# Optimization experiments

Measured on AMD Instinct MI355X. Metric: run time of the kernel, lower is better.

The kernel has to match this reference:

```python
import jax, jax.numpy as jnp
import numpy as np

# dims matching input_specs / init_kwargs
S_BATCH, T_BATCH, NUM, DIM, H, W = 4, 4, 8, 512, 32, 32
K = 64              # self.k, number of kmeans clusters
KMEANS_ITERS = 10   # fixed Lloyd iterations (stand-in for kmeans-to-convergence)


def _kmeans(points):
    """Euclidean Lloyd kmeans. points: [n, d] -> centers [K, d].
    Deterministic init: first K points. Empty clusters keep old center."""
    centers0 = points[:K]
    sq_p = jnp.sum(points * points, axis=1)  # [n]

    def step(centers, _):
        # squared euclidean distance [n, K]
        d2 = sq_p[:, None] + jnp.sum(centers * centers, axis=1)[None, :] \
             - 2.0 * points @ centers.T
        assign = jnp.argmin(d2, axis=1)                      # [n]
        onehot = jax.nn.one_hot(assign, K, dtype=points.dtype)  # [n, K]
        counts = onehot.sum(axis=0)                          # [K]
        sums = onehot.T @ points                             # [K, d]
        new = jnp.where(counts[:, None] > 0,
                        sums / jnp.maximum(counts, 1.0)[:, None],
                        centers)
        return new, None

    centers, _ = jax.lax.scan(step, centers0, None, length=KMEANS_ITERS)
    return centers


def setup_inputs() -> dict:
    key = jax.random.key(0)
    k1, k2, k3, k4 = jax.random.split(key, 4)
    return {
        "source_feat": jax.random.normal(k1, (S_BATCH, NUM, DIM, H, W), dtype=jnp.float32),
        "target_feat": jax.random.normal(k2, (T_BATCH, NUM, DIM, H, W), dtype=jnp.float32),
        "source_label": jax.random.randint(k3, (S_BATCH,), 0, 10),
        "target_label": jax.random.randint(k4, (T_BATCH,), 0, 10),
    }


def reference(source_feat, target_feat, source_label, target_label):
    sb, num, dim, h, w = source_feat.shape
    tb = target_feat.shape[0]

    # view each map as (h*w, dim) point cloud, kmeans per (batch, num)
    s_pts = source_feat.reshape(sb, num, dim, h * w).transpose(0, 1, 3, 2)
    t_pts = target_feat.reshape(tb, num, dim, h * w).transpose(0, 1, 3, 2)
    km = jax.vmap(jax.vmap(_kmeans))
    cs = km(s_pts).transpose(1, 0, 2, 3)  # [num, sb, K, dim]
    ct = km(t_pts).transpose(1, 0, 2, 3)  # [num, tb, K, dim]

    # mat_dist for every (num, i, j) pair of center sets: [num, sb, tb, K, K]
    sq_s = jnp.sum(cs * cs, axis=-1)  # [num, sb, K]
    sq_t = jnp.sum(ct * ct, axis=-1)  # [num, tb, K]
    dots = jnp.einsum('nikd,njld->nijkl', cs, ct)
    dist = jnp.sqrt(jnp.maximum(
        sq_s[:, :, None, :, None] + sq_t[:, None, :, None, :] - 2.0 * dots, 0.0))
    y = jnp.argmin(dist, axis=-1)  # [num, sb, tb, K] nearest target center per source center

    # gather matched target centers; replicate source centers over j (torch append order: i, j, k)
    ct_b = jnp.broadcast_to(ct[:, None], (num, sb, tb, K, dim))
    t_mat = jnp.take_along_axis(ct_b, y[..., None], axis=3)            # [num, sb, tb, K, dim]
    s_mat = jnp.broadcast_to(cs[:, :, None], (num, sb, tb, K, dim))

    N = sb * tb * K
    s_mat = s_mat.reshape(num, N, dim)
    t_mat = t_mat.reshape(num, N, dim)

    # trans_mat[k] = s_mat.T @ pinv(t_mat.T)   -> [num, dim, dim]
    pinv_t = jnp.linalg.pinv(t_mat.transpose(0, 2, 1))  # pinv([dim, N]) -> [num, N, dim]
    trans_mat = jnp.einsum('nkd,nke->nde', s_mat, pinv_t)
    return trans_mat
```

## Files before the change

kernel.cpp:

```cpp
#include <hip/hip_runtime.h>

typedef unsigned int u32;
typedef unsigned long long u64;

#define NPTS  1024
#define DIMD  512
#define KCL   64
#define KMIT  10

constexpr size_t O_CTG  = 0;
constexpr size_t O_SUMS = O_CTG  + 64ull*512*64;
constexpr size_t O_CNT  = O_SUMS + 64ull*64*512;
constexpr size_t O_SQC  = O_CNT  + 64ull*64;
constexpr size_t O_SQP  = O_SQC  + 64ull*64;
constexpr size_t O_ASG  = O_SQP  + 64ull*1024;
constexpr size_t O_CTN  = O_ASG  + 64ull*1024;
constexpr size_t O_Y    = O_CTN  + 8ull*256*512;
constexpr size_t O_CNT2 = O_Y    + 8ull*4*4*64;
constexpr size_t O_BM   = O_CNT2 + 8ull*256;
constexpr size_t O_G    = O_BM   + 8ull*256*512;
constexpr size_t O_LT   = O_G    + 8ull*256*256;
constexpr size_t O_YB   = O_LT   + 8ull*256*256;
constexpr size_t O_ZB   = O_YB   + 8ull*256*512;
constexpr size_t O_PTST = O_ZB   + 8ull*256*512;

constexpr size_t O_PS0 = O_SUMS;
constexpr size_t O_PS1 = O_CTN;
static_assert(O_PS1 + 64ull*64*512 <= O_G, "PS1 overlay must fit before O_G");

constexpr size_t O_BEST = O_G;

constexpr size_t O_CS = O_SUMS;
constexpr size_t O_W  = O_YB;
constexpr size_t O_WT = O_YB + 8ull*4*64*64;

__device__ __forceinline__ const float* run_base(const float* s, const float* t, int run){
    const float* b = (run < 32) ? s : t;
    return b + (size_t)(run & 31) * (DIMD * NPTS);
}
__device__ __forceinline__ u64 dpack(float d2, int c){
    u32 u = __float_as_uint(d2);
    u = (u & 0x80000000u) ? ~u : (u | 0x80000000u);
    return ((u64)u << 32) | (u32)c;
}
__device__ __forceinline__ float rdlane(float v, int l){
    return __uint_as_float(__builtin_amdgcn_readlane(__float_as_uint(v), l));
}

__global__ __launch_bounds__(256) void k_init(const float* __restrict__ src, const float* __restrict__ tgt,
                                              float* __restrict__ ws){
    int bx = blockIdx.x; int run = bx >> 2, q = bx & 3;
    int tid = threadIdx.x;
    const float* base = run_base(src, tgt, run);
    int p = q*256 + tid;
    float acc = 0.f;
    for (int d = 0; d < DIMD; ++d){
        float v = base[(size_t)d*NPTS + p];
        acc = fmaf(v, v, acc);
    }
    ws[O_SQP + run*NPTS + p] = acc;
    if (q == 0){
        if (tid < KCL) ws[O_SQC + run*KCL + tid] = acc;
        if (tid < KCL) ((int*)(ws + O_CNT))[run*KCL + tid] = 0;
        for (int idx = tid; idx < DIMD*KCL; idx += 256){
            int d = idx >> 6, c = idx & 63;
            ws[O_CTG + (size_t)run*DIMD*KCL + idx] = base[(size_t)d*NPTS + c];
        }
    }
}

__global__ __launch_bounds__(256) void k_ptsT(const float* __restrict__ src, const float* __restrict__ tgt,
                                              float* __restrict__ ws){
    int bx = blockIdx.x; int dt = bx & 7, pt = (bx >> 3) & 15, run = bx >> 7;
    int tid = threadIdx.x, lane = tid & 63, r4 = tid >> 6;
    const float* base = run_base(src, tgt, run);
    __shared__ float t[64*65];
    for (int pass = 0; pass < 16; ++pass){
        int r = pass*4 + r4;
        t[r*65 + lane] = base[(size_t)(dt*64 + r)*NPTS + pt*64 + lane];
    }
    __syncthreads();
    for (int pass = 0; pass < 16; ++pass){
        int p = pass*4 + r4;
        ws[O_PTST + ((size_t)run*NPTS + pt*64 + p)*DIMD + dt*64 + lane] = t[lane*65 + p];
    }
}

__global__ __launch_bounds__(256, 4) void k_assign(const float* __restrict__ src, const float* __restrict__ tgt,
                                                   const float* __restrict__ ctr, const float* __restrict__ sqc,
                                                   const float* __restrict__ sqp,
                                                   u64* __restrict__ bestg){
    int bxx = blockIdx.x;
    int cb  = (bxx >> 3) & 1;
    int w   = ((bxx >> 4) << 3) | (bxx & 7);
    int run = w >> 3, qt = w & 7;
    int tid = threadIdx.x, lane = tid & 63;
    int g = __builtin_amdgcn_readfirstlane(tid >> 6);
    int c0 = cb*32 + g*8;
    const float* base = run_base(src, tgt, run);
    const float* cg = ctr + (size_t)run*DIMD*KCL + c0;
    int p0 = qt*128 + 2*lane;
    float acc[2][8] = {};
    __shared__ u64 red[4][128];

#define LOADP(P, B) { \
    _Pragma("unroll") \
    for (int u = 0; u < 16; ++u) \
        P[u] = *(const float2*)&base[(size_t)((B)*16 + u)*NPTS + p0]; }

#define COMPUTE(P, B) { \
    _Pragma("unroll") \
    for (int u = 0; u < 16; ++u){ \
        const float4* cp = (const float4*)(cg + (size_t)((B)*16 + u)*KCL); \
        float4 c0v = cp[0], c1v = cp[1]; \
        float cv[8] = {c0v.x,c0v.y,c0v.z,c0v.w, c1v.x,c1v.y,c1v.z,c1v.w}; \
        _Pragma("unroll") \
        for (int cl = 0; cl < 8; ++cl){ \
            acc[0][cl] = fmaf(P[u].x, cv[cl], acc[0][cl]); \
            acc[1][cl] = fmaf(P[u].y, cv[cl], acc[1][cl]); \
        } \
    } }

    float2 pa[16], pb[16];
    LOADP(pa, 0);
    for (int b = 0; b < 32; b += 2){
        if (b + 1 < 32) LOADP(pb, b + 1);
        COMPUTE(pa, b);
        if (b + 2 < 32) LOADP(pa, b + 2);
        COMPUTE(pb, b + 1);
    }
#undef LOADP
#undef COMPUTE

    const float* sqcg = sqc + run*KCL + c0;
    float sq[8];
    #pragma unroll
    for (int q = 0; q < 8; ++q) sq[q] = sqcg[q];
    float2 sq2 = *(const float2*)&sqp[run*NPTS + p0];
    #pragma unroll
    for (int s = 0; s < 2; ++s){
        float sqpv = s ? sq2.y : sq2.x;
        u64 best = dpack(sqpv + sq[0] - 2.f*acc[s][0], c0);
        #pragma unroll
        for (int cl = 1; cl < 8; ++cl){
            u64 k2 = dpack(sqpv + sq[cl] - 2.f*acc[s][cl], c0 + cl);
            best = (k2 < best) ? k2 : best;
        }
        red[g][2*lane + s] = best;
    }
    __syncthreads();
    if (tid < 128){
        u64 b = red[0][tid];
        #pragma unroll
        for (int g2 = 1; g2 < 4; ++g2){ u64 k2 = red[g2][tid]; b = (k2 < b) ? k2 : b; }
        bestg[(((size_t)(run*8 + qt)*128 + tid) << 1) + cb] = b;
    }
}

__global__ __launch_bounds__(256) void k_sums(float* __restrict__ ws){
    int bx = blockIdx.x; int pg = bx & 1, dh = (bx >> 1) & 1, run = bx >> 2;
    int tid = threadIdx.x;
    __shared__ float sm[KCL*256];
    __shared__ int a[512];
    const u64* bestg = (const u64*)(ws + O_BEST);
    int* cnt = (int*)(ws + O_CNT);
    for (int idx = tid; idx < 512; idx += 256){
        int p = pg*512 + idx;
        int qt = p >> 7, t = p & 127;
        const u64* bp = bestg + (((size_t)(run*8 + qt)*128 + t) << 1);
        u64 x = bp[0], y = bp[1];
        u64 m = (y < x) ? y : x;
        int c = (int)(m & 0xffffffffu);
        a[idx] = c;
        if (dh == 0) atomicAdd(&cnt[run*KCL + c], 1);
    }
    for (int idx = tid; idx < KCL*256; idx += 256) sm[idx] = 0.f;
    __syncthreads();
    const float* pT = ws + O_PTST + ((size_t)run*NPTS + pg*512)*DIMD + dh*256 + tid;
    for (int p = 0; p < 512; p += 4){
        float v0 = pT[(size_t)(p+0)*DIMD], v1 = pT[(size_t)(p+1)*DIMD];
        float v2 = pT[(size_t)(p+2)*DIMD], v3 = pT[(size_t)(p+3)*DIMD];
        sm[a[p+0]*256 + tid] += v0;
        sm[a[p+1]*256 + tid] += v1;
        sm[a[p+2]*256 + tid] += v2;
        sm[a[p+3]*256 + tid] += v3;
    }
    __syncthreads();
    size_t psx = pg ? O_PS1 : O_PS0;
    for (int c = 0; c < KCL; ++c)
        ws[psx + ((size_t)run*KCL + c)*DIMD + dh*256 + tid] = sm[c*256 + tid];
}

__global__ __launch_bounds__(256) void k_newc(float* __restrict__ ws){
    int run = blockIdx.x, tid = threadIdx.x;
    __shared__ float sm2[KCL*65];
    __shared__ int cl[KCL];
    int* cnt = (int*)(ws + O_CNT);
    if (tid < KCL) cl[tid] = cnt[run*KCL + tid];
    __syncthreads();
    if (tid < KCL) cnt[run*KCL + tid] = 0;
    float sqa = 0.f;
    for (int dc = 0; dc < 8; ++dc){
        for (int idx = tid; idx < KCL*64; idx += 256){
            int c = idx >> 6, dl = idx & 63;
            size_t o = ((size_t)run*KCL + c)*DIMD + dc*64 + dl;
            sm2[c*65 + dl] = ws[O_PS0 + o] + ws[O_PS1 + o];
        }
        __syncthreads();
        for (int idx = tid; idx < KCL*64; idx += 256){
            int dl = idx >> 6, c = idx & 63, d = dc*64 + dl;
            size_t gi = O_CTG + (size_t)run*DIMD*KCL + d*KCL + c;
            float old = ws[gi];
            int cc = cl[c];
            float nv = (cc > 0) ? sm2[c*65 + dl] / (float)cc : old;
            ws[gi] = nv;
            sm2[c*65 + dl] = nv;
        }
        __syncthreads();
        if (tid < KCL){
            for (int dl = 0; dl < 64; ++dl){ float v = sm2[tid*65 + dl]; sqa = fmaf(v, v, sqa); }
        }
        __syncthreads();
    }
    if (tid < KCL) ws[O_SQC + run*KCL + tid] = sqa;
}

__global__ __launch_bounds__(256) void k_ctn(float* __restrict__ ws){
    int bx = blockIdx.x; int dc = bx & 7, jj = (bx >> 3) & 3, n = (bx >> 5) & 7, st = bx >> 8;
    int run = st ? (jj*8 + n) : (32 + jj*8 + n);
    int tid = threadIdx.x, lane = tid & 63, r4 = tid >> 6;
    __shared__ float t[64*65];
    for (int pass = 0; pass < 16; ++pass){
        int r = pass*4 + r4;
        t[r*65 + lane] = ws[O_CTG + (size_t)run*DIMD*KCL + (dc*64 + r)*KCL + lane];
    }
    __syncthreads();
    size_t dstbase = st ? (O_CS  + ((size_t)(n*4 + jj)*64)*DIMD)
                        : (O_CTN + ((size_t)n*256 + jj*64)*DIMD);
    for (int pass = 0; pass < 16; ++pass){
        int l = pass*4 + r4;
        ws[dstbase + (size_t)l*DIMD + dc*64 + lane] = t[lane*65 + l];
    }
}

__global__ __launch_bounds__(256) void k_map(float* __restrict__ ws){
    int bx = blockIdx.x; int j = bx & 3, i = (bx >> 2) & 3, n = bx >> 4;
    int run_s = i*8 + n, run_t = 32 + j*8 + n;
    int tid = threadIdx.x, lane = tid & 63;
    int g = __builtin_amdgcn_readfirstlane(tid >> 6);
    const float* cgs = ws + O_CTG + (size_t)run_s*DIMD*KCL + lane;
    const float* cgt = ws + O_CTG + (size_t)run_t*DIMD*KCL + g*16;
    float acc[16] = {};
    for (int d = 0; d < DIMD; ++d){
        float csv = cgs[d*KCL];
        const float4* cp = (const float4*)(cgt + d*KCL);
        float4 c0=cp[0], c1=cp[1], c2=cp[2], c3=cp[3];
        float cv[16] = {c0.x,c0.y,c0.z,c0.w, c1.x,c1.y,c1.z,c1.w,
                        c2.x,c2.y,c2.z,c2.w, c3.x,c3.y,c3.z,c3.w};
        #pragma unroll
        for (int cl = 0; cl < 16; ++cl) acc[cl] = fmaf(csv, cv[cl], acc[cl]);
    }
    float sqs = ws[O_SQC + run_s*KCL + lane];
    const float* sqtp = ws + O_SQC + run_t*KCL + g*16;
    u64 best = dpack(sqs + sqtp[0] - 2.f*acc[0], g*16);
    #pragma unroll
    for (int cl = 1; cl < 16; ++cl){
        u64 k2 = dpack(sqs + sqtp[cl] - 2.f*acc[cl], g*16 + cl);
        best = (k2 < best) ? k2 : best;
    }
    __shared__ u64 red[4][64];
    red[g][lane] = best;
    __syncthreads();
    if (tid < 64){
        u64 b = red[0][tid];
        #pragma unroll
        for (int g2 = 1; g2 < 4; ++g2){ u64 k2 = red[g2][tid]; b = (k2 < b) ? k2 : b; }
        int l = (int)(b & 0xffffffffu);
        int* yv   = (int*)(ws + O_Y);
        int* cnt2 = (int*)(ws + O_CNT2);
        yv[((n*4 + i)*4 + j)*64 + tid] = l;
        atomicAdd(&cnt2[n*256 + j*64 + l], 1);
    }
}

__global__ __launch_bounds__(256) void k_bmat(float* __restrict__ ws){
    int bx = blockIdx.x; int dh = bx & 1, j = (bx >> 1) & 3, n = bx >> 3;
    int tid = threadIdx.x;
    __shared__ float Bacc[KCL*256];
    __shared__ int yl[256];
    __shared__ int c2[KCL];
    const int* yv   = (const int*)(ws + O_Y);
    const int* cnt2 = (const int*)(ws + O_CNT2);
    { int i = tid >> 6, k = tid & 63; yl[tid] = yv[((n*4 + i)*4 + j)*64 + k]; }
    if (tid < KCL) c2[tid] = cnt2[n*256 + j*64 + tid];
    for (int idx = tid; idx < KCL*256; idx += 256) Bacc[idx] = 0.f;
    __syncthreads();
    const float* cs = ws + O_CS + (size_t)(n*4)*64*DIMD + dh*256 + tid;
    #pragma unroll 4
    for (int s = 0; s < 256; ++s){
        int l = yl[s];
        float v = cs[(size_t)s*DIMD];
        Bacc[l*256 + tid] += v;
    }
    __syncthreads();
    for (int l = 0; l < KCL; ++l){
        int cc = c2[l]; if (cc < 1) cc = 1;
        ws[O_BM + ((size_t)n*256 + j*64 + l)*DIMD + dh*256 + tid] = Bacc[l*256 + tid] / (float)cc;
    }
}

__global__ __launch_bounds__(256) void k_gram(float* __restrict__ ws){
    int bx = blockIdx.x; int cc = bx & 7, n = bx >> 3;
    int tid = threadIdx.x, llane = tid & 63, jlane = tid >> 6;
    int run_t = 32 + jlane*8 + n;
    const float* bbase = ws + O_CTG + (size_t)run_t*DIMD*KCL + llane;
    const float* arow  = ws + O_CTN + (size_t)(n*256 + cc*32)*DIMD;
    float acc[32] = {};
    for (int d = 0; d < DIMD; d += 4){
        float bv0 = bbase[(d+0)*KCL], bv1 = bbase[(d+1)*KCL];
        float bv2 = bbase[(d+2)*KCL], bv3 = bbase[(d+3)*KCL];
        #pragma unroll
        for (int c = 0; c < 32; ++c){
            const float4 av = *(const float4*)&arow[c*DIMD + d];
            acc[c] = fmaf(av.x, bv0, acc[c]);
            acc[c] = fmaf(av.y, bv1, acc[c]);
            acc[c] = fmaf(av.z, bv2, acc[c]);
            acc[c] = fmaf(av.w, bv3, acc[c]);
        }
    }
    const int* cnt2 = (const int*)(ws + O_CNT2);
    bool used_cp = cnt2[n*256 + tid] > 0;
    float* Gp = ws + O_G + (size_t)n*65536;
    #pragma unroll
    for (int c = 0; c < 32; ++c){
        int cg = cc*32 + c;
        bool used_c = cnt2[n*256 + cg] > 0;
        float v = (used_c && used_cp) ? acc[c] : ((cg == tid) ? 1.f : 0.f);
        Gp[(size_t)cg*256 + tid] = v;
    }
}

__global__ __launch_bounds__(256, 1) void k_cholp(float* __restrict__ ws, int kb){
    int n = blockIdx.x, tid = threadIdx.x;
    int lane = tid & 63, wv = tid >> 6;
    float* Gn  = ws + O_G  + (size_t)n*65536;
    float* LTn = ws + O_LT + (size_t)n*65536;
    int c0 = kb*64, r1 = c0 + 64, rem = 256 - r1;

    float dreg[64];
    {
        const float* grow = Gn + (size_t)(c0+lane)*256 + c0;
        #pragma unroll
        for (int j4 = 0; j4 < 16; ++j4){
            float4 v = *(const float4*)&grow[j4*4];
            dreg[j4*4+0]=v.x; dreg[j4*4+1]=v.y; dreg[j4*4+2]=v.z; dreg[j4*4+3]=v.w;
        }
    }
    float preg[64];
    int prow = (wv-1)*64 + lane;
    bool pact = (wv >= 1) && (prow < rem);
    {
        const float* growp = Gn + (size_t)(r1+prow)*256 + c0;
        #pragma unroll
        for (int j4 = 0; j4 < 16; ++j4){
            if (pact){
                float4 v = *(const float4*)&growp[j4*4];
                preg[j4*4+0]=v.x; preg[j4*4+1]=v.y; preg[j4*4+2]=v.z; preg[j4*4+3]=v.w;
            } else {
                preg[j4*4+0]=0.f; preg[j4*4+1]=0.f; preg[j4*4+2]=0.f; preg[j4*4+3]=0.f;
            }
        }
    }
    #pragma unroll
    for (int k = 0; k < 64; ++k){
        float dkk = sqrtf(fmaxf(rdlane(dreg[k], k), 1e-30f));
        float inv = 1.f / dkk;
        dreg[k] = (lane == k) ? dkk : dreg[k]*inv;
        preg[k] *= inv;
        #pragma unroll
        for (int j = k+1; j < 64; ++j){
            float s = rdlane(dreg[k], j);
            dreg[j] = fmaf(-dreg[k], s, dreg[j]);
            preg[j] = fmaf(-preg[k], s, preg[j]);
        }
    }
    if (wv == 0){
        float* grow = Gn + (size_t)(c0+lane)*256 + c0;
        #pragma unroll
        for (int j4 = 0; j4 < 16; ++j4){
            float4 v; v.x=dreg[j4*4+0]; v.y=dreg[j4*4+1]; v.z=dreg[j4*4+2]; v.w=dreg[j4*4+3];
            *(float4*)&grow[j4*4] = v;
        }
    }
    if (pact){
        float* growp = Gn + (size_t)(r1+prow)*256 + c0;
        #pragma unroll
        for (int j4 = 0; j4 < 16; ++j4){
            float4 v; v.x=preg[j4*4+0]; v.y=preg[j4*4+1]; v.z=preg[j4*4+2]; v.w=preg[j4*4+3];
            *(float4*)&growp[j4*4] = v;
        }
        float* ltp = LTn + (size_t)c0*256 + r1 + prow;
        #pragma unroll
        for (int j = 0; j < 64; ++j) ltp[(size_t)j*256] = preg[j];
    }
}

__global__ __launch_bounds__(256) void k_trail(float* __restrict__ ws, int kb){
    int n = blockIdx.y;
    int c0 = kb*64, r1 = c0 + 64, rem = 256 - r1;
    int nt4 = rem >> 2;
    int ntiles = nt4*(nt4+1)/2;
    float* Gn = ws + O_G + (size_t)n*65536;
    for (int t = blockIdx.x*256 + threadIdx.x; t < ntiles; t += gridDim.x*256){
        int ti = (int)((sqrtf(8.f*(float)t + 1.f) - 1.f) * 0.5f);
        while ((ti+1)*(ti+2)/2 <= t) ++ti;
        while (ti*(ti+1)/2 > t) --ti;
        int tj = t - ti*(ti+1)/2;
        int i0 = ti*4, j0 = tj*4;
        const float* Li = Gn + (size_t)(r1+i0)*256 + c0;
        const float* Lj = Gn + (size_t)(r1+j0)*256 + c0;
        float acc[4][4] = {};
        for (int k = 0; k < 64; k += 4){
            float4 ar4[4], br4[4];
            #pragma unroll
            for (int r = 0; r < 4; ++r) ar4[r] = *(const float4*)&Li[(size_t)r*256 + k];
            #pragma unroll
            for (int s = 0; s < 4; ++s) br4[s] = *(const float4*)&Lj[(size_t)s*256 + k];
            #pragma unroll
            for (int q = 0; q < 4; ++q){
                float aq[4] = { q==0?ar4[0].x:q==1?ar4[0].y:q==2?ar4[0].z:ar4[0].w,
                                q==0?ar4[1].x:q==1?ar4[1].y:q==2?ar4[1].z:ar4[1].w,
                                q==0?ar4[2].x:q==1?ar4[2].y:q==2?ar4[2].z:ar4[2].w,
                                q==0?ar4[3].x:q==1?ar4[3].y:q==2?ar4[3].z:ar4[3].w };
                float bq[4] = { q==0?br4[0].x:q==1?br4[0].y:q==2?br4[0].z:br4[0].w,
                                q==0?br4[1].x:q==1?br4[1].y:q==2?br4[1].z:br4[1].w,
                                q==0?br4[2].x:q==1?br4[2].y:q==2?br4[2].z:br4[2].w,
                                q==0?br4[3].x:q==1?br4[3].y:q==2?br4[3].z:br4[3].w };
                #pragma unroll
                for (int r = 0; r < 4; ++r)
                    #pragma unroll
                    for (int s = 0; s < 4; ++s)
                        acc[r][s] = fmaf(aq[r], bq[s], acc[r][s]);
            }
        }
        #pragma unroll
        for (int r = 0; r < 4; ++r){
            float* grow = Gn + (size_t)(r1+i0+r)*256 + r1 + j0;
            #pragma unroll
            for (int s = 0; s < 4; ++s) grow[s] -= acc[r][s];
        }
    }
}

__global__ __launch_bounds__(256, 1) void k_dinv(float* __restrict__ ws){
    int n = blockIdx.x, tid = threadIdx.x;
    int lane = tid & 63, kb = tid >> 6;
    const float* Gn = ws + O_G + (size_t)n*65536;
    __shared__ __align__(16) float DlT[4][64*65];
    for (int idx = lane; idx < 1024; idx += 64){
        int r = idx >> 4, c4 = idx & 15;
        float4 v = *(const float4*)&Gn[(size_t)(kb*64 + r)*256 + kb*64 + c4*4];
        DlT[kb][(c4*4+0)*65 + r] = v.x;
        DlT[kb][(c4*4+1)*65 + r] = v.y;
        DlT[kb][(c4*4+2)*65 + r] = v.z;
        DlT[kb][(c4*4+3)*65 + r] = v.w;
    }
    __syncthreads();
    float x[64];
    #pragma unroll
    for (int i = 0; i < 64; ++i) x[i] = (i == lane) ? 1.f : 0.f;
    const float* Dk = DlT[kb];
    #pragma unroll
    for (int k = 0; k < 64; ++k){
        float invd = 1.f / Dk[k*65 + k];
        x[k] *= invd;
        #pragma unroll
        for (int i = k+1; i < 64; ++i)
            x[i] = fmaf(-Dk[k*65 + i], x[k], x[i]);
    }
    float* Wg  = ws + O_W  + ((size_t)n*4 + kb)*4096;
    float* WTg = ws + O_WT + ((size_t)n*4 + kb)*4096;
    #pragma unroll
    for (int r = 0; r < 64; ++r) Wg[r*64 + lane] = x[r];
    #pragma unroll
    for (int r4 = 0; r4 < 16; ++r4){
        float4 v; v.x=x[r4*4+0]; v.y=x[r4*4+1]; v.z=x[r4*4+2]; v.w=x[r4*4+3];
        *(float4*)&WTg[lane*64 + r4*4] = v;
    }
}

__global__ __launch_bounds__(256, 1) void k_solve(float* __restrict__ ws){
    int n = blockIdx.x, cg = blockIdx.y;
    int tid = threadIdx.x;
    int tx = tid & 15, ty = tid >> 4;
    const float* Gn  = ws + O_G  + (size_t)n*65536;
    const float* LTn = ws + O_LT + (size_t)n*65536;
    const float* Ct  = ws + O_CTN + (size_t)n*256*DIMD + (size_t)cg*64;
    const float* Wg  = ws + O_W  + (size_t)n*4*4096;
    const float* WTg = ws + O_WT + (size_t)n*4*4096;
    float* Zb = ws + O_ZB + (size_t)n*256*DIMD + (size_t)cg*64;

    __shared__ __align__(16) float YL[4][64*65];
    __shared__ __align__(16) float At[64*65];
    __shared__ __align__(16) float RL[64*65];

    float acc[4][4];
    for (int bi = 0; bi < 4; ++bi){
        #pragma unroll
        for (int a = 0; a < 4; ++a){
            float4 v = *(const float4*)&Ct[(size_t)(bi*64 + ty*4 + a)*DIMD + tx*4];
            acc[a][0]=v.x; acc[a][1]=v.y; acc[a][2]=v.z; acc[a][3]=v.w;
        }
        for (int j = 0; j < bi; ++j){
            __syncthreads();
            for (int idx = tid; idx < 1024; idx += 256){
                int k = idx >> 4, r4 = idx & 15;
                float4 v = *(const float4*)&LTn[(size_t)(j*64 + k)*256 + bi*64 + r4*4];
                *(float4*)&At[k*65 + r4*4] = v;
            }
            __syncthreads();
            const float* Yj = YL[j];
            #pragma unroll 8
            for (int k = 0; k < 64; ++k){
                float4 av = *(const float4*)&At[k*65 + ty*4];
                float4 yv = *(const float4*)&Yj[k*65 + tx*4];
                float ar[4] = {av.x,av.y,av.z,av.w};
                float yr[4] = {yv.x,yv.y,yv.z,yv.w};
                #pragma unroll
                for (int a = 0; a < 4; ++a)
                    #pragma unroll
                    for (int b = 0; b < 4; ++b)
                        acc[a][b] = fmaf(-ar[a], yr[b], acc[a][b]);
            }
        }
        __syncthreads();
        #pragma unroll
        for (int a = 0; a < 4; ++a){
            float4 v; v.x=acc[a][0]; v.y=acc[a][1]; v.z=acc[a][2]; v.w=acc[a][3];
            *(float4*)&RL[(ty*4 + a)*65 + tx*4] = v;
        }
        for (int idx = tid; idx < 1024; idx += 256){
            int k = idx >> 4, r4 = idx & 15;
            float4 v = *(const float4*)&WTg[(size_t)bi*4096 + k*64 + r4*4];
            *(float4*)&At[k*65 + r4*4] = v;
        }
        __syncthreads();
        float out[4][4] = {};
        #pragma unroll 8
        for (int k = 0; k < 64; ++k){
            float4 av = *(const float4*)&At[k*65 + ty*4];
            float4 rv = *(const float4*)&RL[k*65 + tx*4];
            float ar[4] = {av.x,av.y,av.z,av.w};
            float rr[4] = {rv.x,rv.y,rv.z,rv.w};
            #pragma unroll
            for (int a = 0; a < 4; ++a)
                #pragma unroll
                for (int b = 0; b < 4; ++b)
                    out[a][b] = fmaf(ar[a], rr[b], out[a][b]);
        }
        float* Yi = YL[bi];
        #pragma unroll
        for (int a = 0; a < 4; ++a){
            float4 v; v.x=out[a][0]; v.y=out[a][1]; v.z=out[a][2]; v.w=out[a][3];
            *(float4*)&Yi[(ty*4 + a)*65 + tx*4] = v;
        }
    }
    for (int bi = 3; bi >= 0; --bi){
        __syncthreads();
        #pragma unroll
        for (int a = 0; a < 4; ++a){
            float4 v = *(const float4*)&YL[bi][(ty*4 + a)*65 + tx*4];
            acc[a][0]=v.x; acc[a][1]=v.y; acc[a][2]=v.z; acc[a][3]=v.w;
        }
        for (int j = bi+1; j < 4; ++j){
            __syncthreads();
            for (int idx = tid; idx < 1024; idx += 256){
                int k = idx >> 4, r4 = idx & 15;
                float4 v = *(const float4*)&Gn[(size_t)(j*64 + k)*256 + bi*64 + r4*4];
                *(float4*)&At[k*65 + r4*4] = v;
            }
            __syncthreads();
            const float* Zj = YL[j];
            #pragma unroll 8
            for (int k = 0; k < 64; ++k){
                float4 av = *(const float4*)&At[k*65 + ty*4];
                float4 zv = *(const float4*)&Zj[k*65 + tx*4];
                float ar[4] = {av.x,av.y,av.z,av.w};
                float zr[4] = {zv.x,zv.y,zv.z,zv.w};
                #pragma unroll
                for (int a = 0; a < 4; ++a)
                    #pragma unroll
                    for (int b = 0; b < 4; ++b)
                        acc[a][b] = fmaf(-ar[a], zr[b], acc[a][b]);
            }
        }
        __syncthreads();
        #pragma unroll
        for (int a = 0; a < 4; ++a){
            float4 v; v.x=acc[a][0]; v.y=acc[a][1]; v.z=acc[a][2]; v.w=acc[a][3];
            *(float4*)&RL[(ty*4 + a)*65 + tx*4] = v;
        }
        for (int idx = tid; idx < 1024; idx += 256){
            int k = idx >> 4, r4 = idx & 15;
            float4 v = *(const float4*)&Wg[(size_t)bi*4096 + k*64 + r4*4];
            *(float4*)&At[k*65 + r4*4] = v;
        }
        __syncthreads();
        float out[4][4] = {};
        #pragma unroll 8
        for (int k = 0; k < 64; ++k){
            float4 av = *(const float4*)&At[k*65 + ty*4];
            float4 rv = *(const float4*)&RL[k*65 + tx*4];
            float ar[4] = {av.x,av.y,av.z,av.w};
            float rr[4] = {rv.x,rv.y,rv.z,rv.w};
            #pragma unroll
            for (int a = 0; a < 4; ++a)
                #pragma unroll
                for (int b = 0; b < 4; ++b)
                    out[a][b] = fmaf(ar[a], rr[b], out[a][b]);
        }
        float* Zi = YL[bi];
        #pragma unroll
        for (int a = 0; a < 4; ++a){
            float4 v; v.x=out[a][0]; v.y=out[a][1]; v.z=out[a][2]; v.w=out[a][3];
            *(float4*)&Zi[(ty*4 + a)*65 + tx*4] = v;
            *(float4*)&Zb[(size_t)(bi*64 + ty*4 + a)*DIMD + tx*4] = v;
        }
    }
}

__global__ __launch_bounds__(256) void k_gemmE(const float* __restrict__ ws, float* __restrict__ out){
    int bx = blockIdx.x; int et = bx & 7, dt = (bx >> 3) & 7, n = bx >> 6;
    int tid = threadIdx.x;
    __shared__ float Bl[256*64];
    __shared__ float Zl[256*64];
    const float* Bm = ws + O_BM + (size_t)n*256*DIMD;
    const float* Zb = ws + O_ZB + (size_t)n*256*DIMD;
    for (int idx = tid; idx < 16384; idx += 256){
        int c = idx >> 6, dd = idx & 63;
        Bl[idx] = Bm[(size_t)c*DIMD + dt*64 + dd];
        Zl[idx] = Zb[(size_t)c*DIMD + et*64 + dd];
    }
    __syncthreads();
    int td = tid & 15, te = tid >> 4;
    float acc[4][4] = {};
    for (int c = 0; c < 256; ++c){
        float4 bv = *(const float4*)&Bl[c*64 + td*4];
        float4 zv = *(const float4*)&Zl[c*64 + te*4];
        float b4[4] = {bv.x, bv.y, bv.z, bv.w};
        float z4[4] = {zv.x, zv.y, zv.z, zv.w};
        #pragma unroll
        for (int r = 0; r < 4; ++r)
            #pragma unroll
            for (int s = 0; s < 4; ++s) acc[r][s] = fmaf(b4[r], z4[s], acc[r][s]);
    }
    float* ob = out + (size_t)n*262144 + (size_t)(dt*64 + td*4)*DIMD + et*64 + te*4;
    #pragma unroll
    for (int r = 0; r < 4; ++r){
        float4 o; o.x = acc[r][0]; o.y = acc[r][1]; o.z = acc[r][2]; o.w = acc[r][3];
        *(float4*)&ob[(size_t)r*DIMD] = o;
    }
}

extern "C" void kernel_launch(void* const* d_in, const int* in_sizes, int n_in,
                              void* d_out, int out_size, void* d_ws, size_t ws_size,
                              hipStream_t stream){
    const float* src = (const float*)d_in[0];
    const float* tgt = (const float*)d_in[1];
    float* ws  = (float*)d_ws;
    float* out = (float*)d_out;

    k_init<<<256, 256, 0, stream>>>(src, tgt, ws);
    k_ptsT<<<8192, 256, 0, stream>>>(src, tgt, ws);

    for (int it = 0; it < KMIT; ++it){
        k_assign<<<1024, 256, 0, stream>>>(src, tgt,
                                           ws + O_CTG, ws + O_SQC, ws + O_SQP,
                                           (u64*)(ws + O_BEST));
        k_sums<<<256, 256, 0, stream>>>(ws);
        k_newc<<<64, 256, 0, stream>>>(ws);
    }

    hipMemsetAsync((char*)d_ws + O_CNT2*4, 0, 8*256*4, stream);
    k_ctn<<<512, 256, 0, stream>>>(ws);
    k_map<<<128, 256, 0, stream>>>(ws);
    k_bmat<<<64, 256, 0, stream>>>(ws);
    k_gram<<<64, 256, 0, stream>>>(ws);
    for (int kb = 0; kb < 4; ++kb){
        k_cholp<<<8, 256, 0, stream>>>(ws, kb);
        if (kb < 3) k_trail<<<dim3(8, 8), 256, 0, stream>>>(ws, kb);
    }
    k_dinv<<<8, 256, 0, stream>>>(ws);
    k_solve<<<dim3(8, 8), 256, 0, stream>>>(ws);
    k_gemmE<<<512, 256, 0, stream>>>(ws, out);
}
```

Baseline: 2.598 ms.

## Tile Gram kernel through LDS and halve k_assign prefetch chunk

k_gram is rewritten as a shared-memory tiled GEMM. Each block now computes a 64x64 tile of the 256x256 Gram matrix from the matched-centre rows, with a 4x4 register micro-tile per thread. It launches 128 blocks instead of 64. This replaces the old per-lane strided reads of the centre matrix with reuse of data staged in LDS. Separately, the point-prefetch chunk in k_assign drops from 16 to 8 dimensions per stage. That is meant to lower register pressure and improve occupancy, at the cost of more loop iterations. The LDS rows use a stride of 65 floats but are written with float4 stores, so alignment of those writes is a risk.

```diff
diff --git a/kernel.cpp b/kernel.cpp
--- a/kernel.cpp
+++ b/kernel.cpp
@@ -103,15 +103,15 @@
     float acc[2][8] = {};
     __shared__ u64 red[4][128];
 
-#define LOADP(P, B) { \
+#define LOADP(P, DB) { \
     _Pragma("unroll") \
-    for (int u = 0; u < 16; ++u) \
-        P[u] = *(const float2*)&base[(size_t)((B)*16 + u)*NPTS + p0]; }
-
-#define COMPUTE(P, B) { \
+    for (int u = 0; u < 8; ++u) \
+        P[u] = *(const float2*)&base[(size_t)((DB)*8 + u)*NPTS + p0]; }
+
+#define COMPUTE(P, DB) { \
     _Pragma("unroll") \
-    for (int u = 0; u < 16; ++u){ \
-        const float4* cp = (const float4*)(cg + (size_t)((B)*16 + u)*KCL); \
+    for (int u = 0; u < 8; ++u){ \
+        const float4* cp = (const float4*)(cg + (size_t)((DB)*8 + u)*KCL); \
         float4 c0v = cp[0], c1v = cp[1]; \
         float cv[8] = {c0v.x,c0v.y,c0v.z,c0v.w, c1v.x,c1v.y,c1v.z,c1v.w}; \
         _Pragma("unroll") \
@@ -121,13 +121,13 @@
         } \
     } }
 
-    float2 pa[16], pb[16];
+    float2 pa[8], pb[8];
     LOADP(pa, 0);
-    for (int b = 0; b < 32; b += 2){
-        if (b + 1 < 32) LOADP(pb, b + 1);
-        COMPUTE(pa, b);
-        if (b + 2 < 32) LOADP(pa, b + 2);
-        COMPUTE(pb, b + 1);
+    for (int db = 0; db < 64; db += 2){
+        if (db + 1 < 64) LOADP(pb, db + 1);
+        COMPUTE(pa, db);
+        if (db + 2 < 64) LOADP(pa, db + 2);
+        COMPUTE(pb, db + 1);
     }
 #undef LOADP
 #undef COMPUTE
@@ -310,33 +310,48 @@
 }
 
 __global__ __launch_bounds__(256) void k_gram(float* __restrict__ ws){
-    int bx = blockIdx.x; int cc = bx & 7, n = bx >> 3;
-    int tid = threadIdx.x, llane = tid & 63, jlane = tid >> 6;
-    int run_t = 32 + jlane*8 + n;
-    const float* bbase = ws + O_CTG + (size_t)run_t*DIMD*KCL + llane;
-    const float* arow  = ws + O_CTN + (size_t)(n*256 + cc*32)*DIMD;
-    float acc[32] = {};
-    for (int d = 0; d < DIMD; d += 4){
-        float bv0 = bbase[(d+0)*KCL], bv1 = bbase[(d+1)*KCL];
-        float bv2 = bbase[(d+2)*KCL], bv3 = bbase[(d+3)*KCL];
-        #pragma unroll
-        for (int c = 0; c < 32; ++c){
-            const float4 av = *(const float4*)&arow[c*DIMD + d];
-            acc[c] = fmaf(av.x, bv0, acc[c]);
-            acc[c] = fmaf(av.y, bv1, acc[c]);
-            acc[c] = fmaf(av.z, bv2, acc[c]);
-            acc[c] = fmaf(av.w, bv3, acc[c]);
+    int bx = blockIdx.x; int ti = bx & 3, tj = (bx >> 2) & 3, n = bx >> 4;
+    int tid = threadIdx.x;
+    int tx = tid & 15, ty = tid >> 4;
+    const float* A = ws + O_CTN + (size_t)n*256*DIMD;
+    __shared__ __align__(16) float Ai[64*65];
+    __shared__ __align__(16) float Aj[64*65];
+    float acc[4][4] = {};
+    for (int kc = 0; kc < 8; ++kc){
+        __syncthreads();
+        for (int idx = tid; idx < 1024; idx += 256){
+            int r = idx >> 4, c4 = idx & 15;
+            *(float4*)&Ai[r*65 + c4*4] = *(const float4*)&A[(size_t)(ti*64 + r)*DIMD + kc*64 + c4*4];
+            *(float4*)&Aj[r*65 + c4*4] = *(const float4*)&A[(size_t)(tj*64 + r)*DIMD + kc*64 + c4*4];
+        }
+        __syncthreads();
+        #pragma unroll 8
+        for (int k = 0; k < 64; ++k){
+            float ar[4], br[4];
+            #pragma unroll
+            for (int a = 0; a < 4; ++a) ar[a] = Ai[(ty*4 + a)*65 + k];
+            #pragma unroll
+            for (int b = 0; b < 4; ++b) br[b] = Aj[(tx*4 + b)*65 + k];
+            #pragma unroll
+            for (int a = 0; a < 4; ++a)
+                #pragma unroll
+                for (int b = 0; b < 4; ++b)
+                    acc[a][b] = fmaf(ar[a], br[b], acc[a][b]);
         }
     }
     const int* cnt2 = (const int*)(ws + O_CNT2);
-    bool used_cp = cnt2[n*256 + tid] > 0;
     float* Gp = ws + O_G + (size_t)n*65536;
     #pragma unroll
-    for (int c = 0; c < 32; ++c){
-        int cg = cc*32 + c;
-        bool used_c = cnt2[n*256 + cg] > 0;
-        float v = (used_c && used_cp) ? acc[c] : ((cg == tid) ? 1.f : 0.f);
-        Gp[(size_t)cg*256 + tid] = v;
+    for (int a = 0; a < 4; ++a){
+        int row = ti*64 + ty*4 + a;
+        bool ur = cnt2[n*256 + row] > 0;
+        #pragma unroll
+        for (int b = 0; b < 4; ++b){
+            int col = tj*64 + tx*4 + b;
+            bool uc = cnt2[n*256 + col] > 0;
+            float v = (ur && uc) ? acc[a][b] : ((row == col) ? 1.f : 0.f);
+            Gp[(size_t)row*256 + col] = v;
+        }
     }
 }
 
@@ -685,7 +700,7 @@
     k_ctn<<<512, 256, 0, stream>>>(ws);
     k_map<<<128, 256, 0, stream>>>(ws);
     k_bmat<<<64, 256, 0, stream>>>(ws);
-    k_gram<<<64, 256, 0, stream>>>(ws);
+    k_gram<<<128, 256, 0, stream>>>(ws);
     for (int kb = 0; kb < 4; ++kb){
         k_cholp<<<8, 256, 0, stream>>>(ws, kb);
         if (kb < 3) k_trail<<<dim3(8, 8), 256, 0, stream>>>(ws, kb);
```

Measured after the change: 2.318 ms. 10.8% less time.
